# Kernel optimization log

Measured on AMD Instinct MI355X. Metric: run time of the kernel, lower is better.

## Reference

```python
import jax, jax.numpy as jnp
import numpy as np

B, T, C, H = 2, 2048, 1024, 16
D = C // H  # head dim = 64

def setup_inputs() -> dict:
    key = jax.random.key(0)
    k1, k2, k3 = jax.random.split(key, 3)
    x = jax.random.normal(k1, (B, T, C), dtype=jnp.float32)
    Wqkv = jax.random.normal(k2, (C, 3 * C), dtype=jnp.float32) * (1.0 / np.sqrt(C))
    bqkv = jnp.zeros((3 * C,), dtype=jnp.float32)
    Wo = jax.random.normal(k3, (C, C), dtype=jnp.float32) * (1.0 / np.sqrt(C))
    bo = jnp.zeros((C,), dtype=jnp.float32)
    return {"x": x, "Wqkv": Wqkv, "bqkv": bqkv, "Wo": Wo, "bo": bo}

def reference(x, Wqkv, bqkv, Wo, bo):
    b, t, c = x.shape
    qkv = x @ Wqkv + bqkv                              # [B,T,3C]
    q, k, v = jnp.split(qkv, 3, axis=-1)
    # [B,T,C] -> [B,H,T,D]
    q = q.reshape(b, t, H, D).transpose(0, 2, 1, 3)
    k = k.reshape(b, t, H, D).transpose(0, 2, 1, 3)
    v = v.reshape(b, t, H, D).transpose(0, 2, 1, 3)
    scores = jnp.einsum('bhqd,bhkd->bhqk', q, k) * (1.0 / np.sqrt(D))
    causal = jnp.tril(jnp.ones((t, t), dtype=bool))
    scores = jnp.where(causal, scores, -jnp.inf)
    probs = jax.nn.softmax(scores, axis=-1)           # dropout p=0 -> identity
    out = jnp.einsum('bhqk,bhkd->bhqd', probs, v)
    out = out.transpose(0, 2, 1, 3).reshape(b, t, c)
    return out @ Wo + bo
```

## Files before the change

kernel.cpp:

```cpp
#include <hip/hip_runtime.h>
#include <hip/hip_bf16.h>

typedef __attribute__((ext_vector_type(8))) short bf16x8;
typedef __attribute__((ext_vector_type(4))) short bf16x4;
typedef __attribute__((ext_vector_type(4))) float f32x4;

static __device__ __forceinline__ __hip_bfloat16 f2b(float f) {
    return __float2bfloat16(f);
}
static __device__ __forceinline__ unsigned pack2(float a, float b) {
    unsigned ua = (unsigned)__bfloat16_as_ushort(__float2bfloat16(a));
    unsigned ub = (unsigned)__bfloat16_as_ushort(__float2bfloat16(b));
    return ua | (ub << 16);
}
static __device__ __forceinline__ float exp2fast(float x) {
    return __builtin_amdgcn_exp2f(x);
}

__global__ __launch_bounds__(256) void k_f32_to_bf16(
    const float* __restrict__ in, __hip_bfloat16* __restrict__ out, int n4)
{
    int i = blockIdx.x * blockDim.x + threadIdx.x;
    int stride = gridDim.x * blockDim.x;
    for (; i < n4; i += stride) {
        float4 v = reinterpret_cast<const float4*>(in)[i];
        __hip_bfloat16* o = out + 4 * (size_t)i;
        o[0] = f2b(v.x); o[1] = f2b(v.y); o[2] = f2b(v.z); o[3] = f2b(v.w);
    }
}

__global__ __launch_bounds__(256) void k_transpose_f32_bf16(
    const float* __restrict__ in, __hip_bfloat16* __restrict__ out, int R, int Cn)
{
    __shared__ float tile[32][33];
    const int c0 = blockIdx.x * 32, r0 = blockIdx.y * 32;
    const int tx = threadIdx.x & 31, ty = threadIdx.x >> 5;
#pragma unroll
    for (int i = 0; i < 32; i += 8)
        tile[ty + i][tx] = in[(size_t)(r0 + ty + i) * Cn + c0 + tx];
    __syncthreads();
#pragma unroll
    for (int i = 0; i < 32; i += 8)
        out[(size_t)(c0 + ty + i) * R + r0 + tx] = f2b(tile[tx][ty + i]);
}

#define QSCALE 0.1803368801111f

#define QK_STAGE(buf, kt)                                                       \
    {                                                                           \
        const int k0_ = (kt) << 5;                                              \
        _Pragma("unroll")                                                       \
        for (int i = 0; i < 2; ++i) {                                           \
            const int idx = i * 256 + tid;                                      \
            const int r_ = idx >> 2;                                            \
            const int j_ = idx & 3;                                             \
            const int js_ = j_ ^ ((r_ >> 1) & 3);                               \
            __builtin_amdgcn_global_load_lds(                                   \
                (const __attribute__((address_space(1))) void*)(A + (size_t)(m0 + r_) * K + k0_ + js_ * 8), \
                (__attribute__((address_space(3))) void*)(&As[buf][r_][j_ * 8]), 16, 0, 0); \
        }                                                                       \
        _Pragma("unroll")                                                       \
        for (int i = 0; i < 2; ++i) {                                           \
            const int idx = i * 256 + tid;                                      \
            const int r_ = idx >> 2;                                            \
            const int j_ = idx & 3;                                             \
            const int js_ = j_ ^ ((r_ >> 1) & 3);                               \
            __builtin_amdgcn_global_load_lds(                                   \
                (const __attribute__((address_space(1))) void*)(Bt + (size_t)(n0 + r_) * K + k0_ + js_ * 8), \
                (__attribute__((address_space(3))) void*)(&Bs[buf][r_][j_ * 8]), 16, 0, 0); \
        }                                                                       \
    }

__global__ __launch_bounds__(256, 3) void k_gemm_qkv(
    const __hip_bfloat16* __restrict__ A,
    const __hip_bfloat16* __restrict__ Bt,
    const float* __restrict__ bias,
    int K,
    __hip_bfloat16* __restrict__ Qb,
    __hip_bfloat16* __restrict__ Kb,
    __hip_bfloat16* __restrict__ Vt)
{
    __shared__ __hip_bfloat16 As[2][128][32];
    __shared__ __hip_bfloat16 Bs[2][128][32];

    const int tid = threadIdx.x;
    const int lane = tid & 63;
    const int wid = tid >> 6;
    const int wm = wid >> 1, wn = wid & 1;
    const int m0 = blockIdx.y * 128, n0 = blockIdx.x * 128;
    const int l15 = lane & 15, lg = lane >> 4;
    const int rchunk = (lg ^ ((l15 >> 1) & 3)) * 8;

    f32x4 acc[4][4] = {};
    const int nt = K >> 5;

    QK_STAGE(0, 0);
    __syncthreads();
    int cur = 0;
    for (int t = 0; t < nt; ++t) {
        if (t + 1 < nt) QK_STAGE(cur ^ 1, t + 1);
        bf16x8 a[4], bb[4];
#pragma unroll
        for (int m = 0; m < 4; ++m)
            a[m] = *(const bf16x8*)&As[cur][wm * 64 + m * 16 + l15][rchunk];
#pragma unroll
        for (int n = 0; n < 4; ++n)
            bb[n] = *(const bf16x8*)&Bs[cur][wn * 64 + n * 16 + l15][rchunk];
        __builtin_amdgcn_s_setprio(1);
#pragma unroll
        for (int m = 0; m < 4; ++m)
#pragma unroll
            for (int n = 0; n < 4; ++n)
                acc[m][n] = __builtin_amdgcn_mfma_f32_16x16x32_bf16(a[m], bb[n], acc[m][n], 0, 0, 0);
        __builtin_amdgcn_s_setprio(0);
        __syncthreads();
        cur ^= 1;
    }

#pragma unroll
    for (int m = 0; m < 4; ++m) {
        const int row = m0 + wm * 64 + m * 16 + lg * 4;
#pragma unroll
        for (int n = 0; n < 4; ++n) {
            const int col = n0 + wn * 64 + n * 16 + l15;
            const float bv = bias[col];
#pragma unroll
            for (int r = 0; r < 4; ++r) {
                const float val = acc[m][n][r] + bv;
                const int rr = row + r;
                const int sec = col >> 10, cw = col & 1023;
                const int hh = cw >> 6, d = cw & 63;
                const int bq = rr >> 11, tt = rr & 2047;
                const int bh = bq * 16 + hh;
                if (sec == 0)
                    Qb[((size_t)bh * 2048 + tt) * 64 + d] = f2b(val * QSCALE);
                else if (sec == 1)
                    Kb[((size_t)bh * 2048 + tt) * 64 + d] = f2b(val);
                else
                    Vt[((size_t)bh * 64 + d) * 2048 + tt] = f2b(val);
            }
        }
    }
}

#define OUT_STAGE(buf, kt)                                                      \
    {                                                                           \
        const int k0_ = (kt) << 5;                                              \
        _Pragma("unroll")                                                       \
        for (int i = 0; i < 2; ++i) {                                           \
            const int idx = i * 256 + tid;                                      \
            const int r_ = idx >> 2;                                            \
            const int j_ = idx & 3;                                             \
            const int js_ = j_ ^ ((r_ >> 1) & 3);                               \
            __builtin_amdgcn_global_load_lds(                                   \
                (const __attribute__((address_space(1))) void*)(A + (size_t)(m0 + r_) * K + k0_ + js_ * 8), \
                (__attribute__((address_space(3))) void*)(&As[buf][r_][j_ * 8]), 16, 0, 0); \
        }                                                                       \
        {                                                                       \
            const int r_ = tid >> 2;                                            \
            const int j_ = tid & 3;                                             \
            const int js_ = j_ ^ ((r_ >> 1) & 3);                               \
            __builtin_amdgcn_global_load_lds(                                   \
                (const __attribute__((address_space(1))) void*)(Bt + (size_t)(n0 + r_) * K + k0_ + js_ * 8), \
                (__attribute__((address_space(3))) void*)(&Bs[buf][r_][j_ * 8]), 16, 0, 0); \
        }                                                                       \
    }

__global__ __launch_bounds__(256, 4) void k_gemm_out(
    const __hip_bfloat16* __restrict__ A,
    const __hip_bfloat16* __restrict__ Bt,
    const float* __restrict__ bias,
    int K, int Nn,
    float* __restrict__ outf)
{
    __shared__ __hip_bfloat16 As[2][128][32];
    __shared__ __hip_bfloat16 Bs[2][64][32];

    const int tid = threadIdx.x;
    const int lane = tid & 63;
    const int wid = tid >> 6;
    const int wm = wid >> 1, wn = wid & 1;
    const int m0 = blockIdx.y * 128, n0 = blockIdx.x * 64;
    const int l15 = lane & 15, lg = lane >> 4;
    const int rchunk = (lg ^ ((l15 >> 1) & 3)) * 8;

    f32x4 acc[4][2] = {};
    const int nt = K >> 5;

    OUT_STAGE(0, 0);
    __syncthreads();
    int cur = 0;
    for (int t = 0; t < nt; ++t) {
        if (t + 1 < nt) OUT_STAGE(cur ^ 1, t + 1);
        bf16x8 a[4], bb[2];
#pragma unroll
        for (int m = 0; m < 4; ++m)
            a[m] = *(const bf16x8*)&As[cur][wm * 64 + m * 16 + l15][rchunk];
#pragma unroll
        for (int n = 0; n < 2; ++n)
            bb[n] = *(const bf16x8*)&Bs[cur][wn * 32 + n * 16 + l15][rchunk];
        __builtin_amdgcn_s_setprio(1);
#pragma unroll
        for (int m = 0; m < 4; ++m)
#pragma unroll
            for (int n = 0; n < 2; ++n)
                acc[m][n] = __builtin_amdgcn_mfma_f32_16x16x32_bf16(a[m], bb[n], acc[m][n], 0, 0, 0);
        __builtin_amdgcn_s_setprio(0);
        __syncthreads();
        cur ^= 1;
    }

#pragma unroll
    for (int m = 0; m < 4; ++m) {
        const int row = m0 + wm * 64 + m * 16 + lg * 4;
#pragma unroll
        for (int n = 0; n < 2; ++n) {
            const int col = n0 + wn * 32 + n * 16 + l15;
            const float bv = bias[col];
#pragma unroll
            for (int r = 0; r < 4; ++r)
                outf[(size_t)(row + r) * Nn + col] = acc[m][n][r] + bv;
        }
    }
}

#define DEFER_THR 4.0f

#define K_LOAD(BK, KS)                                                          \
    {                                                                           \
        _Pragma("unroll")                                                       \
        for (int kf = 0; kf < 4; ++kf) {                                        \
            const __hip_bfloat16* kp =                                          \
                Kbase + (size_t)((KS) + kf * 16 + l15) * 64 + lg * 8;           \
            BK[kf][0] = *(const bf16x8*)(kp);                                   \
            BK[kf][1] = *(const bf16x8*)(kp + 32);                              \
        }                                                                       \
    }

#define FULL_STEP(BK, BKN, KS)                                                  \
    {                                                                           \
        const int ks_ = (KS);                                                   \
        bf16x8 bv[4][2];                                                        \
        _Pragma("unroll")                                                       \
        for (int dc = 0; dc < 4; ++dc) {                                        \
            const __hip_bfloat16* vp =                                          \
                Vbase + (size_t)(dc * 16 + l15) * 2048 + ks_ + lg * 8;          \
            bv[dc][0] = *(const bf16x8*)(vp);                                   \
            bv[dc][1] = *(const bf16x8*)(vp + 32);                              \
        }                                                                       \
        K_LOAD(BKN, ks_ + 64);                                                  \
        f32x4 s0[4] = {}, s1[4] = {};                                           \
        __builtin_amdgcn_s_setprio(1);                                          \
        _Pragma("unroll")                                                       \
        for (int kf = 0; kf < 4; ++kf) {                                        \
            s0[kf] = __builtin_amdgcn_mfma_f32_16x16x32_bf16(BK[kf][0], aq[0][0], s0[kf], 0, 0, 0); \
            s0[kf] = __builtin_amdgcn_mfma_f32_16x16x32_bf16(BK[kf][1], aq[0][1], s0[kf], 0, 0, 0); \
            s1[kf] = __builtin_amdgcn_mfma_f32_16x16x32_bf16(BK[kf][0], aq[1][0], s1[kf], 0, 0, 0); \
            s1[kf] = __builtin_amdgcn_mfma_f32_16x16x32_bf16(BK[kf][1], aq[1][1], s1[kf], 0, 0, 0); \
        }                                                                       \
        __builtin_amdgcn_s_setprio(0);                                          \
        float px0 = fmaxf(fmaxf(fmaxf(s0[0][0], s0[0][1]), fmaxf(s0[0][2], s0[0][3])), \
                          fmaxf(fmaxf(s0[1][0], s0[1][1]), fmaxf(s0[1][2], s0[1][3]))); \
        px0 = fmaxf(px0, fmaxf(fmaxf(fmaxf(s0[2][0], s0[2][1]), fmaxf(s0[2][2], s0[2][3])), \
                               fmaxf(fmaxf(s0[3][0], s0[3][1]), fmaxf(s0[3][2], s0[3][3])))); \
        float px1 = fmaxf(fmaxf(fmaxf(s1[0][0], s1[0][1]), fmaxf(s1[0][2], s1[0][3])), \
                          fmaxf(fmaxf(s1[1][0], s1[1][1]), fmaxf(s1[1][2], s1[1][3]))); \
        px1 = fmaxf(px1, fmaxf(fmaxf(fmaxf(s1[2][0], s1[2][1]), fmaxf(s1[2][2], s1[2][3])), \
                               fmaxf(fmaxf(s1[3][0], s1[3][1]), fmaxf(s1[3][2], s1[3][3])))); \
        px0 = fmaxf(px0, __shfl_xor(px0, 16));                                  \
        px0 = fmaxf(px0, __shfl_xor(px0, 32));                                  \
        px1 = fmaxf(px1, __shfl_xor(px1, 16));                                  \
        px1 = fmaxf(px1, __shfl_xor(px1, 32));                                  \
        if (__any((px0 > m0 + DEFER_THR) || (px1 > m1 + DEFER_THR))) {          \
            const float mn0 = fmaxf(m0, px0), mn1 = fmaxf(m1, px1);             \
            const float al0 = exp2fast(m0 - mn0), al1 = exp2fast(m1 - mn1);     \
            m0 = mn0; m1 = mn1;                                                 \
            l0 *= al0; l1 *= al1;                                               \
            _Pragma("unroll")                                                   \
            for (int dc = 0; dc < 4; ++dc)                                      \
                _Pragma("unroll")                                               \
                for (int r = 0; r < 4; ++r) {                                   \
                    o[0][dc][r] *= al0;                                         \
                    o[1][dc][r] *= al1;                                         \
                }                                                               \
        }                                                                       \
        float rs0 = 0.f, rs1 = 0.f;                                             \
        _Pragma("unroll")                                                       \
        for (int kf = 0; kf < 4; ++kf) {                                        \
            _Pragma("unroll")                                                   \
            for (int r = 0; r < 4; ++r) {                                       \
                s0[kf][r] = exp2fast(s0[kf][r] - m0);                           \
                s1[kf][r] = exp2fast(s1[kf][r] - m1);                           \
                rs0 += s0[kf][r];                                               \
                rs1 += s1[kf][r];                                               \
            }                                                                   \
            uint2 w0, w1;                                                       \
            w0.x = pack2(s0[kf][0], s0[kf][1]); w0.y = pack2(s0[kf][2], s0[kf][3]); \
            w1.x = pack2(s1[kf][0], s1[kf][1]); w1.y = pack2(s1[kf][2], s1[kf][3]); \
            const int off = l15 * 64 + ((kf * 16 + lg * 4) ^ swz);              \
            *(uint2*)&Pw0[off] = w0;                                            \
            *(uint2*)&Pw1[off] = w1;                                            \
        }                                                                       \
        rs0 += __shfl_xor(rs0, 16); rs0 += __shfl_xor(rs0, 32);                 \
        rs1 += __shfl_xor(rs1, 16); rs1 += __shfl_xor(rs1, 32);                 \
        l0 += rs0; l1 += rs1;                                                   \
        _Pragma("unroll")                                                       \
        for (int c2 = 0; c2 < 2; ++c2) {                                        \
            const int off = l15 * 64 + ((c2 * 32 + lg * 8) ^ swz);              \
            const bf16x8 pb0 = *(const bf16x8*)&Pw0[off];                       \
            const bf16x8 pb1 = *(const bf16x8*)&Pw1[off];                       \
            __builtin_amdgcn_s_setprio(1);                                      \
            _Pragma("unroll")                                                   \
            for (int dc = 0; dc < 4; ++dc) {                                    \
                o[0][dc] = __builtin_amdgcn_mfma_f32_16x16x32_bf16(bv[dc][c2], pb0, o[0][dc], 0, 0, 0); \
                o[1][dc] = __builtin_amdgcn_mfma_f32_16x16x32_bf16(bv[dc][c2], pb1, o[1][dc], 0, 0, 0); \
            }                                                                   \
            __builtin_amdgcn_s_setprio(0);                                      \
        }                                                                       \
    }

#define TAIL_STEP(BK)                                                           \
    {                                                                           \
        const int ks_ = nfull * 64;                                             \
        bf16x8 bv[4][2];                                                        \
        _Pragma("unroll")                                                       \
        for (int dc = 0; dc < 4; ++dc) {                                        \
            const __hip_bfloat16* vp =                                          \
                Vbase + (size_t)(dc * 16 + l15) * 2048 + ks_ + lg * 8;          \
            bv[dc][0] = *(const bf16x8*)(vp);                                   \
            bv[dc][1] = *(const bf16x8*)(vp + 32);                              \
        }                                                                       \
        float mr[2] = {m0, m1}, lr[2] = {l0, l1};                               \
        _Pragma("unroll")                                                       \
        for (int qf = 0; qf < 2; ++qf) {                                        \
            const int qlo = qw + qf * 16;                                       \
            const int qv = qlo + l15;                                           \
            f32x4 s[4] = {};                                                    \
            _Pragma("unroll")                                                   \
            for (int kf = 0; kf < 4; ++kf) {                                    \
                if (ks_ + kf * 16 <= qlo + 15) {                                \
                    s[kf] = __builtin_amdgcn_mfma_f32_16x16x32_bf16(BK[kf][0], aq[qf][0], s[kf], 0, 0, 0); \
                    s[kf] = __builtin_amdgcn_mfma_f32_16x16x32_bf16(BK[kf][1], aq[qf][1], s[kf], 0, 0, 0); \
                }                                                               \
            }                                                                   \
            float p[4][4];                                                      \
            const int kb = ks_ + lg * 4;                                        \
            _Pragma("unroll")                                                   \
            for (int kf = 0; kf < 4; ++kf)                                      \
                _Pragma("unroll")                                               \
                for (int r = 0; r < 4; ++r)                                     \
                    p[kf][r] = (kb + kf * 16 + r <= qv) ? s[kf][r] : -1e30f;    \
            float mx = fmaxf(fmaxf(fmaxf(p[0][0], p[0][1]), fmaxf(p[0][2], p[0][3])), \
                             fmaxf(fmaxf(p[1][0], p[1][1]), fmaxf(p[1][2], p[1][3]))); \
            mx = fmaxf(mx, fmaxf(fmaxf(fmaxf(p[2][0], p[2][1]), fmaxf(p[2][2], p[2][3])), \
                                 fmaxf(fmaxf(p[3][0], p[3][1]), fmaxf(p[3][2], p[3][3])))); \
            mx = fmaxf(mx, __shfl_xor(mx, 16));                                 \
            mx = fmaxf(mx, __shfl_xor(mx, 32));                                 \
            const float mnew = fmaxf(mr[qf], mx);                               \
            const float al = exp2fast(mr[qf] - mnew);                           \
            mr[qf] = mnew;                                                      \
            float rs = 0.f;                                                     \
            _Pragma("unroll")                                                   \
            for (int kf = 0; kf < 4; ++kf)                                      \
                _Pragma("unroll")                                               \
                for (int r = 0; r < 4; ++r) {                                   \
                    p[kf][r] = exp2fast(p[kf][r] - mnew);                       \
                    rs += p[kf][r];                                             \
                }                                                               \
            rs += __shfl_xor(rs, 16);                                           \
            rs += __shfl_xor(rs, 32);                                           \
            lr[qf] = lr[qf] * al + rs;                                          \
            _Pragma("unroll")                                                   \
            for (int dc = 0; dc < 4; ++dc)                                      \
                _Pragma("unroll")                                               \
                for (int r = 0; r < 4; ++r) o[qf][dc][r] *= al;                 \
            __hip_bfloat16* Pw = (qf == 0) ? Pw0 : Pw1;                         \
            _Pragma("unroll")                                                   \
            for (int kf = 0; kf < 4; ++kf) {                                    \
                uint2 w;                                                        \
                w.x = pack2(p[kf][0], p[kf][1]);                                \
                w.y = pack2(p[kf][2], p[kf][3]);                                \
                *(uint2*)&Pw[l15 * 64 + ((kf * 16 + lg * 4) ^ swz)] = w;        \
            }                                                                   \
            _Pragma("unroll")                                                   \
            for (int c2 = 0; c2 < 2; ++c2) {                                    \
                if (ks_ + c2 * 32 <= qlo + 15) {                                \
                    const bf16x8 pb = *(const bf16x8*)&Pw[l15 * 64 + ((c2 * 32 + lg * 8) ^ swz)]; \
                    _Pragma("unroll")                                           \
                    for (int dc = 0; dc < 4; ++dc)                              \
                        o[qf][dc] = __builtin_amdgcn_mfma_f32_16x16x32_bf16(bv[dc][c2], pb, o[qf][dc], 0, 0, 0); \
                }                                                               \
            }                                                                   \
        }                                                                       \
        l0 = lr[0]; l1 = lr[1];                                                 \
    }

__global__ __launch_bounds__(256, 2) void k_attn(
    const __hip_bfloat16* __restrict__ Qb,
    const __hip_bfloat16* __restrict__ Kb,
    const __hip_bfloat16* __restrict__ Vt,
    __hip_bfloat16* __restrict__ att)
{
    __shared__ __hip_bfloat16 P_lds[4][2][16 * 64];
    const int tid = threadIdx.x, lane = tid & 63, wid = tid >> 6;
    const int lid = blockIdx.x;
    const int xcd = lid & 7, j = lid >> 3;
    const int jj = j >> 2;
    const int tile = (jj < 8) ? (15 - jj) : (jj - 8);
    const int bh = xcd * 4 + (j & 3);
    const int q0 = tile * 128;
    const int qw = q0 + wid * 32;
    const int l15 = lane & 15, lg = lane >> 4;
    const int swz = (l15 & 7) << 3;

    const __hip_bfloat16* Qbase = Qb + (size_t)bh * 2048 * 64;
    const __hip_bfloat16* Kbase = Kb + (size_t)bh * 2048 * 64;
    const __hip_bfloat16* Vbase = Vt + (size_t)bh * 64 * 2048;

    bf16x8 aq[2][2];
#pragma unroll
    for (int qf = 0; qf < 2; ++qf)
#pragma unroll
        for (int c = 0; c < 2; ++c)
            aq[qf][c] = *(const bf16x8*)(Qbase + (size_t)(qw + qf * 16 + l15) * 64 + c * 32 + lg * 8);

    f32x4 o[2][4] = {};
    float m0 = -1e30f, m1 = -1e30f, l0 = 0.f, l1 = 0.f;

    const int nfull = qw >> 6;
    __hip_bfloat16* Pw0 = &P_lds[wid][0][0];
    __hip_bfloat16* Pw1 = &P_lds[wid][1][0];

    bf16x8 bkA[4][2], bkB[4][2];
    K_LOAD(bkA, 0);

    if (nfull & 1) {
        FULL_STEP(bkA, bkB, 0);
        for (int t = 1; t < nfull; t += 2) {
            FULL_STEP(bkB, bkA, t * 64);
            FULL_STEP(bkA, bkB, (t + 1) * 64);
        }
        TAIL_STEP(bkB);
    } else {
        for (int t = 0; t < nfull; t += 2) {
            FULL_STEP(bkA, bkB, t * 64);
            FULL_STEP(bkB, bkA, (t + 1) * 64);
        }
        TAIL_STEP(bkA);
    }

    const int bq = bh >> 4, hh = bh & 15;
    const float inv0 = 1.0f / l0, inv1 = 1.0f / l1;
#pragma unroll
    for (int qf = 0; qf < 2; ++qf) {
        const float inv = (qf == 0) ? inv0 : inv1;
        const size_t rowb = ((size_t)(bq * 2048 + qw + qf * 16 + l15)) * 1024 + hh * 64;
#pragma unroll
        for (int dc = 0; dc < 4; ++dc) {
            bf16x4 st;
#pragma unroll
            for (int r = 0; r < 4; ++r)
                st[r] = (short)__bfloat16_as_ushort(__float2bfloat16(o[qf][dc][r] * inv));
            *(bf16x4*)(att + rowb + dc * 16 + lg * 4) = st;
        }
    }
}

extern "C" void kernel_launch(void* const* d_in, const int* in_sizes, int n_in,
                              void* d_out, int out_size, void* d_ws, size_t ws_size,
                              hipStream_t stream)
{
    const float* x    = (const float*)d_in[0];
    const float* Wqkv = (const float*)d_in[1];
    const float* bqkv = (const float*)d_in[2];
    const float* Wo   = (const float*)d_in[3];
    const float* bo   = (const float*)d_in[4];
    float* out = (float*)d_out;

    char* ws = (char*)d_ws;
    const size_t MB = 1024 * 1024;
    __hip_bfloat16* xb    = (__hip_bfloat16*)(ws);
    __hip_bfloat16* WqkvT = (__hip_bfloat16*)(ws + 8 * MB);
    __hip_bfloat16* WoT   = (__hip_bfloat16*)(ws + 14 * MB);
    __hip_bfloat16* Qb    = (__hip_bfloat16*)(ws + 16 * MB);
    __hip_bfloat16* Kb    = (__hip_bfloat16*)(ws + 24 * MB);
    __hip_bfloat16* Vt    = (__hip_bfloat16*)(ws + 32 * MB);
    __hip_bfloat16* att   = (__hip_bfloat16*)(ws + 40 * MB);

    k_f32_to_bf16<<<2048, 256, 0, stream>>>(x, xb, 4096 * 1024 / 4);
    k_transpose_f32_bf16<<<dim3(96, 32), 256, 0, stream>>>(Wqkv, WqkvT, 1024, 3072);
    k_transpose_f32_bf16<<<dim3(32, 32), 256, 0, stream>>>(Wo, WoT, 1024, 1024);

    k_gemm_qkv<<<dim3(24, 32), 256, 0, stream>>>(
        xb, WqkvT, bqkv, 1024, Qb, Kb, Vt);

    k_attn<<<512, 256, 0, stream>>>(Qb, Kb, Vt, att);

    k_gemm_out<<<dim3(16, 32), 256, 0, stream>>>(
        att, WoT, bo, 1024, 1024, out);
}
```

Before: 140.2 us.

## Split attention KV range across two wave groups and merge via LDS

Doubles the attention block to 512 threads, with two wave groups each handling half of the key range for the same query rows: group 1 takes the later half plus the diagonal tail, group 0 the earlier full tiles. Group 1 writes its partial O, max and sum to shared memory, and after a barrier group 0 rescales and merges the two partials before writing the output. This shortens each wave's serial KV loop and raises waves per CU. The cost is extra LDS for the partials, a block-wide sync, and the merge arithmetic. Group 0 gets no tail step, so the two halves can be uneven.

```diff
diff --git a/kernel.cpp b/kernel.cpp
--- a/kernel.cpp
+++ b/kernel.cpp
@@ -392,24 +392,28 @@
                 }                                                               \
             }                                                                   \
         }                                                                       \
+        m0 = mr[0]; m1 = mr[1];                                                 \
         l0 = lr[0]; l1 = lr[1];                                                 \
     }
 
-__global__ __launch_bounds__(256, 2) void k_attn(
+__global__ __launch_bounds__(512, 3) void k_attn(
     const __hip_bfloat16* __restrict__ Qb,
     const __hip_bfloat16* __restrict__ Kb,
     const __hip_bfloat16* __restrict__ Vt,
     __hip_bfloat16* __restrict__ att)
 {
-    __shared__ __hip_bfloat16 P_lds[4][2][16 * 64];
+    __shared__ __hip_bfloat16 P_lds[8][2][16 * 64];
+    __shared__ float Mo[4][64][33];
+    __shared__ float Mml[4][64][5];
     const int tid = threadIdx.x, lane = tid & 63, wid = tid >> 6;
+    const int role = wid >> 2, qsub = wid & 3;
     const int lid = blockIdx.x;
     const int xcd = lid & 7, j = lid >> 3;
     const int jj = j >> 2;
     const int tile = (jj < 8) ? (15 - jj) : (jj - 8);
     const int bh = xcd * 4 + (j & 3);
     const int q0 = tile * 128;
-    const int qw = q0 + wid * 32;
+    const int qw = q0 + qsub * 32;
     const int l15 = lane & 15, lg = lane >> 4;
     const int swz = (l15 & 7) << 3;
 
@@ -428,40 +432,88 @@
     float m0 = -1e30f, m1 = -1e30f, l0 = 0.f, l1 = 0.f;
 
     const int nfull = qw >> 6;
+    const int nA = nfull >> 1;
     __hip_bfloat16* Pw0 = &P_lds[wid][0][0];
     __hip_bfloat16* Pw1 = &P_lds[wid][1][0];
 
     bf16x8 bkA[4][2], bkB[4][2];
-    K_LOAD(bkA, 0);
-
-    if (nfull & 1) {
-        FULL_STEP(bkA, bkB, 0);
-        for (int t = 1; t < nfull; t += 2) {
-            FULL_STEP(bkB, bkA, t * 64);
-            FULL_STEP(bkA, bkB, (t + 1) * 64);
+
+    if (role == 0) {
+        if (nA > 0) {
+            K_LOAD(bkA, 0);
+            if (nA & 1) {
+                FULL_STEP(bkA, bkB, 0);
+                for (int t = 1; t < nA; t += 2) {
+                    FULL_STEP(bkB, bkA, t * 64);
+                    FULL_STEP(bkA, bkB, (t + 1) * 64);
+                }
+            } else {
+                for (int t = 0; t < nA; t += 2) {
+                    FULL_STEP(bkA, bkB, t * 64);
+                    FULL_STEP(bkB, bkA, (t + 1) * 64);
+                }
+            }
         }
-        TAIL_STEP(bkB);
     } else {
-        for (int t = 0; t < nfull; t += 2) {
-            FULL_STEP(bkA, bkB, t * 64);
-            FULL_STEP(bkB, bkA, (t + 1) * 64);
+        const int ksB = nA * 64;
+        const int nB = nfull - nA;
+        K_LOAD(bkA, ksB);
+        if (nB & 1) {
+            FULL_STEP(bkA, bkB, ksB);
+            for (int t = 1; t < nB; t += 2) {
+                FULL_STEP(bkB, bkA, ksB + t * 64);
+                FULL_STEP(bkA, bkB, ksB + (t + 1) * 64);
+            }
+            TAIL_STEP(bkB);
+        } else {
+            for (int t = 0; t < nB; t += 2) {
+                FULL_STEP(bkA, bkB, ksB + t * 64);
+                FULL_STEP(bkB, bkA, ksB + (t + 1) * 64);
+            }
+            TAIL_STEP(bkA);
         }
-        TAIL_STEP(bkA);
-    }
-
-    const int bq = bh >> 4, hh = bh & 15;
-    const float inv0 = 1.0f / l0, inv1 = 1.0f / l1;
-#pragma unroll
-    for (int qf = 0; qf < 2; ++qf) {
-        const float inv = (qf == 0) ? inv0 : inv1;
-        const size_t rowb = ((size_t)(bq * 2048 + qw + qf * 16 + l15)) * 1024 + hh * 64;
-#pragma unroll
-        for (int dc = 0; dc < 4; ++dc) {
-            bf16x4 st;
-#pragma unroll
-            for (int r = 0; r < 4; ++r)
-                st[r] = (short)__bfloat16_as_ushort(__float2bfloat16(o[qf][dc][r] * inv));
-            *(bf16x4*)(att + rowb + dc * 16 + lg * 4) = st;
+#pragma unroll
+        for (int qf = 0; qf < 2; ++qf)
+#pragma unroll
+            for (int dc = 0; dc < 4; ++dc)
+#pragma unroll
+                for (int r = 0; r < 4; ++r)
+                    Mo[qsub][lane][qf * 16 + dc * 4 + r] = o[qf][dc][r];
+        Mml[qsub][lane][0] = m0;
+        Mml[qsub][lane][1] = m1;
+        Mml[qsub][lane][2] = l0;
+        Mml[qsub][lane][3] = l1;
+    }
+
+    __syncthreads();
+
+    if (role == 0) {
+        const float mB0 = Mml[qsub][lane][0], mB1 = Mml[qsub][lane][1];
+        const float lB0 = Mml[qsub][lane][2], lB1 = Mml[qsub][lane][3];
+        const float mf0 = fmaxf(m0, mB0), mf1 = fmaxf(m1, mB1);
+        const float aA0 = exp2fast(m0 - mf0), aB0 = exp2fast(mB0 - mf0);
+        const float aA1 = exp2fast(m1 - mf1), aB1 = exp2fast(mB1 - mf1);
+        const float inv0 = 1.0f / (l0 * aA0 + lB0 * aB0);
+        const float inv1 = 1.0f / (l1 * aA1 + lB1 * aB1);
+
+        const int bq = bh >> 4, hh = bh & 15;
+#pragma unroll
+        for (int qf = 0; qf < 2; ++qf) {
+            const float inv = (qf == 0) ? inv0 : inv1;
+            const float aA = (qf == 0) ? aA0 : aA1;
+            const float aB = (qf == 0) ? aB0 : aB1;
+            const size_t rowb = ((size_t)(bq * 2048 + qw + qf * 16 + l15)) * 1024 + hh * 64;
+#pragma unroll
+            for (int dc = 0; dc < 4; ++dc) {
+                bf16x4 st;
+#pragma unroll
+                for (int r = 0; r < 4; ++r) {
+                    const float ob = Mo[qsub][lane][qf * 16 + dc * 4 + r];
+                    const float val = (o[qf][dc][r] * aA + ob * aB) * inv;
+                    st[r] = (short)__bfloat16_as_ushort(__float2bfloat16(val));
+                }
+                *(bf16x4*)(att + rowb + dc * 16 + lg * 4) = st;
+            }
         }
     }
 }
@@ -494,7 +546,7 @@
     k_gemm_qkv<<<dim3(24, 32), 256, 0, stream>>>(
         xb, WqkvT, bqkv, 1024, Qb, Kb, Vt);
 
-    k_attn<<<512, 256, 0, stream>>>(Qb, Kb, Vt, att);
+    k_attn<<<512, 512, 0, stream>>>(Qb, Kb, Vt, att);
 
     k_gemm_out<<<dim3(16, 32), 256, 0, stream>>>(
         att, WoT, bo, 1024, 1024, out);
```

After: 208.4 us. 1.49x slower.

## Split attention KV range across two blocks and merge partials

Applied to the files above, without the earlier changes.

Each query tile's key range is split into two halves handled by separate blocks (grid doubled to 1024). Each block writes an unnormalized partial output plus its running max and sum, and a new merge kernel combines the two halves and rescales them into the attention output. The aim is more parallelism and better load balance across CUs for the causal workload. In exchange it adds an extra kernel launch, extra global traffic for the partials, and an extra bf16 rounding of the unnormalized partial outputs before the merge.

```diff
diff --git a/kernel.cpp b/kernel.cpp
--- a/kernel.cpp
+++ b/kernel.cpp
@@ -15,6 +15,12 @@
 }
 static __device__ __forceinline__ float exp2fast(float x) {
     return __builtin_amdgcn_exp2f(x);
+}
+static __device__ __forceinline__ float b2f(short u) {
+    unsigned ub = ((unsigned)(unsigned short)u) << 16;
+    float f;
+    __builtin_memcpy(&f, &ub, 4);
+    return f;
 }
 
 __global__ __launch_bounds__(256) void k_f32_to_bf16(
@@ -392,6 +398,7 @@
                 }                                                               \
             }                                                                   \
         }                                                                       \
+        m0 = mr[0]; m1 = mr[1];                                                 \
         l0 = lr[0]; l1 = lr[1];                                                 \
     }
 
@@ -399,15 +406,19 @@
     const __hip_bfloat16* __restrict__ Qb,
     const __hip_bfloat16* __restrict__ Kb,
     const __hip_bfloat16* __restrict__ Vt,
-    __hip_bfloat16* __restrict__ att)
+    __hip_bfloat16* __restrict__ att,
+    __hip_bfloat16* __restrict__ Po,
+    float* __restrict__ Pml)
 {
     __shared__ __hip_bfloat16 P_lds[4][2][16 * 64];
     const int tid = threadIdx.x, lane = tid & 63, wid = tid >> 6;
     const int lid = blockIdx.x;
     const int xcd = lid & 7, j = lid >> 3;
-    const int jj = j >> 2;
-    const int tile = (jj < 8) ? (15 - jj) : (jj - 8);
     const int bh = xcd * 4 + (j & 3);
+    const int u = j >> 2;
+    const int half = u & 1;
+    const int ti = u >> 1;
+    const int tile = (ti < 8) ? (15 - ti) : (ti - 8);
     const int q0 = tile * 128;
     const int qw = q0 + wid * 32;
     const int l15 = lane & 15, lg = lane >> 4;
@@ -428,42 +439,95 @@
     float m0 = -1e30f, m1 = -1e30f, l0 = 0.f, l1 = 0.f;
 
     const int nfull = qw >> 6;
+    const int nA = nfull >> 1;
+    const int kstart = half ? nA * 64 : 0;
+    const int nsteps = half ? (nfull - nA) : nA;
     __hip_bfloat16* Pw0 = &P_lds[wid][0][0];
     __hip_bfloat16* Pw1 = &P_lds[wid][1][0];
 
     bf16x8 bkA[4][2], bkB[4][2];
-    K_LOAD(bkA, 0);
-
-    if (nfull & 1) {
-        FULL_STEP(bkA, bkB, 0);
-        for (int t = 1; t < nfull; t += 2) {
-            FULL_STEP(bkB, bkA, t * 64);
-            FULL_STEP(bkA, bkB, (t + 1) * 64);
+    K_LOAD(bkA, kstart);
+
+    if (nsteps & 1) {
+        FULL_STEP(bkA, bkB, kstart);
+        for (int t = 1; t < nsteps; t += 2) {
+            FULL_STEP(bkB, bkA, kstart + t * 64);
+            FULL_STEP(bkA, bkB, kstart + (t + 1) * 64);
         }
-        TAIL_STEP(bkB);
+        if (half) TAIL_STEP(bkB);
     } else {
-        for (int t = 0; t < nfull; t += 2) {
-            FULL_STEP(bkA, bkB, t * 64);
-            FULL_STEP(bkB, bkA, (t + 1) * 64);
+        for (int t = 0; t < nsteps; t += 2) {
+            FULL_STEP(bkA, bkB, kstart + t * 64);
+            FULL_STEP(bkB, bkA, kstart + (t + 1) * 64);
         }
-        TAIL_STEP(bkA);
-    }
-
-    const int bq = bh >> 4, hh = bh & 15;
-    const float inv0 = 1.0f / l0, inv1 = 1.0f / l1;
-#pragma unroll
-    for (int qf = 0; qf < 2; ++qf) {
-        const float inv = (qf == 0) ? inv0 : inv1;
-        const size_t rowb = ((size_t)(bq * 2048 + qw + qf * 16 + l15)) * 1024 + hh * 64;
-#pragma unroll
-        for (int dc = 0; dc < 4; ++dc) {
-            bf16x4 st;
-#pragma unroll
-            for (int r = 0; r < 4; ++r)
-                st[r] = (short)__bfloat16_as_ushort(__float2bfloat16(o[qf][dc][r] * inv));
-            *(bf16x4*)(att + rowb + dc * 16 + lg * 4) = st;
+        if (half) TAIL_STEP(bkA);
+    }
+
+    if (half == 0) {
+        const int bq = bh >> 4, hh = bh & 15;
+#pragma unroll
+        for (int qf = 0; qf < 2; ++qf) {
+            const int qrow = qw + qf * 16 + l15;
+            const size_t rowb = ((size_t)(bq * 2048 + qrow)) * 1024 + hh * 64;
+#pragma unroll
+            for (int dc = 0; dc < 4; ++dc) {
+                bf16x4 st;
+#pragma unroll
+                for (int r = 0; r < 4; ++r)
+                    st[r] = (short)__bfloat16_as_ushort(__float2bfloat16(o[qf][dc][r]));
+                *(bf16x4*)(att + rowb + dc * 16 + lg * 4) = st;
+            }
+            if (lg == 0) {
+                float2 ml;
+                ml.x = (qf == 0) ? m0 : m1;
+                ml.y = (qf == 0) ? l0 : l1;
+                ((float2*)Pml)[(size_t)bh * 2048 + qrow] = ml;
+            }
         }
-    }
+    } else {
+#pragma unroll
+        for (int qf = 0; qf < 2; ++qf) {
+            const size_t prow = (size_t)bh * 2048 + qw + qf * 16 + l15;
+#pragma unroll
+            for (int dc = 0; dc < 4; ++dc) {
+                bf16x4 st;
+#pragma unroll
+                for (int r = 0; r < 4; ++r)
+                    st[r] = (short)__bfloat16_as_ushort(__float2bfloat16(o[qf][dc][r]));
+                *(bf16x4*)(Po + prow * 64 + dc * 16 + lg * 4) = st;
+            }
+            if (lg == 0) {
+                float2 ml;
+                ml.x = (qf == 0) ? m0 : m1;
+                ml.y = (qf == 0) ? l0 : l1;
+                ((float2*)Pml)[65536 + prow] = ml;
+            }
+        }
+    }
+}
+
+__global__ __launch_bounds__(256) void k_attn_merge(
+    const __hip_bfloat16* __restrict__ Po,
+    const float* __restrict__ Pml,
+    __hip_bfloat16* __restrict__ att)
+{
+    const int idx = blockIdx.x * 256 + threadIdx.x;
+    const int row = idx >> 3, seg = idx & 7;
+    const float2 mlA = ((const float2*)Pml)[row];
+    const float2 mlB = ((const float2*)Pml)[65536 + row];
+    const float mf = fmaxf(mlA.x, mlB.x);
+    const float aA = exp2fast(mlA.x - mf), aB = exp2fast(mlB.x - mf);
+    const float inv = 1.0f / (mlA.y * aA + mlB.y * aB);
+    const float fA = aA * inv, fB = aB * inv;
+    const int bh = row >> 11, qrow = row & 2047;
+    __hip_bfloat16* dst = att + ((size_t)((bh >> 4) * 2048 + qrow) * 1024 + (bh & 15) * 64 + seg * 8);
+    const bf16x8 oa = *(const bf16x8*)dst;
+    const bf16x8 ob = *(const bf16x8*)(Po + (size_t)row * 64 + seg * 8);
+    bf16x8 st;
+#pragma unroll
+    for (int i = 0; i < 8; ++i)
+        st[i] = (short)__bfloat16_as_ushort(f2b(b2f(oa[i]) * fA + b2f(ob[i]) * fB));
+    *(bf16x8*)dst = st;
 }
 
 extern "C" void kernel_launch(void* const* d_in, const int* in_sizes, int n_in,
@@ -486,6 +550,8 @@
     __hip_bfloat16* Kb    = (__hip_bfloat16*)(ws + 24 * MB);
     __hip_bfloat16* Vt    = (__hip_bfloat16*)(ws + 32 * MB);
     __hip_bfloat16* att   = (__hip_bfloat16*)(ws + 40 * MB);
+    __hip_bfloat16* Po    = (__hip_bfloat16*)(ws);
+    float*          Pml   = (float*)(ws + 8 * MB);
 
     k_f32_to_bf16<<<2048, 256, 0, stream>>>(x, xb, 4096 * 1024 / 4);
     k_transpose_f32_bf16<<<dim3(96, 32), 256, 0, stream>>>(Wqkv, WqkvT, 1024, 3072);
@@ -494,7 +560,9 @@
     k_gemm_qkv<<<dim3(24, 32), 256, 0, stream>>>(
         xb, WqkvT, bqkv, 1024, Qb, Kb, Vt);
 
-    k_attn<<<512, 256, 0, stream>>>(Qb, Kb, Vt, att);
+    k_attn<<<1024, 256, 0, stream>>>(Qb, Kb, Vt, att, Po, Pml);
+
+    k_attn_merge<<<2048, 256, 0, stream>>>(Po, Pml, att);
 
     k_gemm_out<<<dim3(16, 32), 256, 0, stream>>>(
         att, WoT, bo, 1024, 1024, out);
```

Result: slower. 158.4 us (+13.0%).

## Merge prep kernels and triple-buffer QKV GEMM with explicit vmcnt waits

Applied to the files above, without the earlier changes.

Folds the x conversion and the two weight transposes into one launch that dispatches on block index, removing two kernel launches. The QKV GEMM moves from double to triple buffering of its LDS tiles, prefetching two stages ahead. It replaces __syncthreads with explicit s_waitcnt vmcnt counts plus s_barrier, so compute can overlap more outstanding global-to-LDS loads. LDS use grows from 32KB to 48KB per block, which may cut occupancy under the 3-blocks launch bound, and the hand-coded vmcnt values must match the number of loads issued per stage.

```diff
diff --git a/kernel.cpp b/kernel.cpp
--- a/kernel.cpp
+++ b/kernel.cpp
@@ -17,23 +17,37 @@
     return __builtin_amdgcn_exp2f(x);
 }
 
-__global__ __launch_bounds__(256) void k_f32_to_bf16(
-    const float* __restrict__ in, __hip_bfloat16* __restrict__ out, int n4)
+#define QSCALE 0.1803368801111f
+
+__global__ __launch_bounds__(256) void k_prep(
+    const float* __restrict__ x, __hip_bfloat16* __restrict__ xb,
+    const float* __restrict__ Wqkv, __hip_bfloat16* __restrict__ WqkvT,
+    const float* __restrict__ Wo, __hip_bfloat16* __restrict__ WoT)
 {
-    int i = blockIdx.x * blockDim.x + threadIdx.x;
-    int stride = gridDim.x * blockDim.x;
-    for (; i < n4; i += stride) {
-        float4 v = reinterpret_cast<const float4*>(in)[i];
-        __hip_bfloat16* o = out + 4 * (size_t)i;
-        o[0] = f2b(v.x); o[1] = f2b(v.y); o[2] = f2b(v.z); o[3] = f2b(v.w);
-    }
-}
-
-__global__ __launch_bounds__(256) void k_transpose_f32_bf16(
-    const float* __restrict__ in, __hip_bfloat16* __restrict__ out, int R, int Cn)
-{
+    const int bx = blockIdx.x;
+    if (bx < 2048) {
+        int i = bx * 256 + threadIdx.x;
+        const int stride = 2048 * 256;
+        for (; i < 1048576; i += stride) {
+            float4 v = reinterpret_cast<const float4*>(x)[i];
+            __hip_bfloat16* o = xb + 4 * (size_t)i;
+            o[0] = f2b(v.x); o[1] = f2b(v.y); o[2] = f2b(v.z); o[3] = f2b(v.w);
+        }
+        return;
+    }
     __shared__ float tile[32][33];
-    const int c0 = blockIdx.x * 32, r0 = blockIdx.y * 32;
+    const float* in;
+    __hip_bfloat16* outp;
+    int R, Cn, c0, r0;
+    if (bx < 5120) {
+        const int b = bx - 2048;
+        in = Wqkv; outp = WqkvT; R = 1024; Cn = 3072;
+        c0 = (b % 96) * 32; r0 = (b / 96) * 32;
+    } else {
+        const int b = bx - 5120;
+        in = Wo; outp = WoT; R = 1024; Cn = 1024;
+        c0 = (b & 31) * 32; r0 = (b >> 5) * 32;
+    }
     const int tx = threadIdx.x & 31, ty = threadIdx.x >> 5;
 #pragma unroll
     for (int i = 0; i < 32; i += 8)
@@ -41,10 +55,8 @@
     __syncthreads();
 #pragma unroll
     for (int i = 0; i < 32; i += 8)
-        out[(size_t)(c0 + ty + i) * R + r0 + tx] = f2b(tile[tx][ty + i]);
-}
-
-#define QSCALE 0.1803368801111f
+        outp[(size_t)(c0 + ty + i) * R + r0 + tx] = f2b(tile[tx][ty + i]);
+}
 
 #define QK_STAGE(buf, kt)                                                       \
     {                                                                           \
@@ -80,8 +92,8 @@
     __hip_bfloat16* __restrict__ Kb,
     __hip_bfloat16* __restrict__ Vt)
 {
-    __shared__ __hip_bfloat16 As[2][128][32];
-    __shared__ __hip_bfloat16 Bs[2][128][32];
+    __shared__ __hip_bfloat16 As[3][128][32];
+    __shared__ __hip_bfloat16 Bs[3][128][32];
 
     const int tid = threadIdx.x;
     const int lane = tid & 63;
@@ -95,10 +107,18 @@
     const int nt = K >> 5;
 
     QK_STAGE(0, 0);
-    __syncthreads();
-    int cur = 0;
+    QK_STAGE(1, 1);
+    asm volatile("s_waitcnt vmcnt(4)" ::: "memory");
+    __builtin_amdgcn_sched_barrier(0);
+    __builtin_amdgcn_s_barrier();
+    __builtin_amdgcn_sched_barrier(0);
+
     for (int t = 0; t < nt; ++t) {
-        if (t + 1 < nt) QK_STAGE(cur ^ 1, t + 1);
+        const int cur = t % 3;
+        if (t + 2 < nt) {
+            const int nxt = (t + 2) % 3;
+            QK_STAGE(nxt, t + 2);
+        }
         bf16x8 a[4], bb[4];
 #pragma unroll
         for (int m = 0; m < 4; ++m)
@@ -113,8 +133,14 @@
             for (int n = 0; n < 4; ++n)
                 acc[m][n] = __builtin_amdgcn_mfma_f32_16x16x32_bf16(a[m], bb[n], acc[m][n], 0, 0, 0);
         __builtin_amdgcn_s_setprio(0);
-        __syncthreads();
-        cur ^= 1;
+        __builtin_amdgcn_sched_barrier(0);
+        if (t + 2 < nt)
+            asm volatile("s_waitcnt vmcnt(4)" ::: "memory");
+        else
+            asm volatile("s_waitcnt vmcnt(0)" ::: "memory");
+        __builtin_amdgcn_sched_barrier(0);
+        __builtin_amdgcn_s_barrier();
+        __builtin_amdgcn_sched_barrier(0);
     }
 
 #pragma unroll
@@ -487,9 +513,7 @@
     __hip_bfloat16* Vt    = (__hip_bfloat16*)(ws + 32 * MB);
     __hip_bfloat16* att   = (__hip_bfloat16*)(ws + 40 * MB);
 
-    k_f32_to_bf16<<<2048, 256, 0, stream>>>(x, xb, 4096 * 1024 / 4);
-    k_transpose_f32_bf16<<<dim3(96, 32), 256, 0, stream>>>(Wqkv, WqkvT, 1024, 3072);
-    k_transpose_f32_bf16<<<dim3(32, 32), 256, 0, stream>>>(Wo, WoT, 1024, 1024);
+    k_prep<<<6144, 256, 0, stream>>>(x, xb, Wqkv, WqkvT, Wo, WoT);
 
     k_gemm_qkv<<<dim3(24, 32), 256, 0, stream>>>(
         xb, WqkvT, bqkv, 1024, Qb, Kb, Vt);
```

Result: faster. 136.5 us (-2.6%).
